# Kernel optimization log

Hardware: AMD Instinct MI355X
Metric: run time of the kernel (lower is better)

The kernel has to match this reference:

```python
import jax, jax.numpy as jnp
import numpy as np

S, N, D, F, E = 2048, 8, 1024, 4096, 8
STD = 0.02


def setup_inputs() -> dict:
    key = jax.random.key(0)
    ks = jax.random.split(key, 5)
    x = jax.random.normal(ks[0], (S, N, D), dtype=jnp.float32)
    Wg = jax.random.normal(ks[1], (E, D), dtype=jnp.float32) * STD
    W1 = jax.random.normal(ks[2], (E, F, D), dtype=jnp.float32) * STD
    b1 = jnp.zeros((E, F), dtype=jnp.float32)
    W2 = jax.random.normal(ks[3], (E, D, F), dtype=jnp.float32) * STD
    b2 = jnp.zeros((E, D), dtype=jnp.float32)
    return {"x": x, "Wg": Wg, "W1": W1, "b1": b1, "W2": W2, "b2": b2}


def reference(x, Wg, W1, b1, W2, b2):
    # Gate (eval mode: no gating noise). scores: [S, N, E]
    scores = jnp.einsum('snd,ed->sne', x, Wg)
    prob = jax.nn.softmax(scores, axis=-1)
    top1_idx = jnp.argmax(prob, axis=-1)                                   # [S, N] int
    top1_prob = jnp.take_along_axis(prob, top1_idx[..., None], axis=-1)[..., 0]  # [S, N]

    y = jnp.zeros_like(x)
    n_experts = Wg.shape[0]
    for e in range(n_experts):  # small fixed loop over experts
        h = jax.nn.gelu(jnp.einsum('snd,fd->snf', x, W1[e]) + b1[e], approximate=False)
        ye = jnp.einsum('snf,df->snd', h, W2[e]) + b2[e]
        mask = (top1_idx == e)[..., None]                                  # [S, N, 1]
        y = y + jnp.where(mask, ye * top1_prob[..., None], 0.0)
    return y
```

## Files before the change

### kernel.cpp

```cpp
#include <hip/hip_runtime.h>

#define S_TOK 16384
#define D_DIM 1024
#define F_DIM 4096
#define E_NUM 8

#define BM 128
#define BN 128
#define BK 64
#define MT_MAX 136

typedef short bf16x8 __attribute__((ext_vector_type(8)));
typedef float f32x4 __attribute__((ext_vector_type(4)));
typedef unsigned short ushort_t;

static __device__ __forceinline__ unsigned short f32_bf16(float f) {
  unsigned u = __float_as_uint(f);
  return (unsigned short)((u + 0x7FFFu + ((u >> 16) & 1u)) >> 16);
}

static __device__ __forceinline__ unsigned int pack_bf16x2(float a, float b) {
  unsigned ua = __float_as_uint(a);
  unsigned ub = __float_as_uint(b);
  unsigned lo = (ua + 0x7FFFu + ((ua >> 16) & 1u)) >> 16;
  unsigned hi = (ub + 0x7FFFu + ((ub >> 16) & 1u)) & 0xFFFF0000u;
  return lo | hi;
}

static __device__ __forceinline__ uint2 cvt_f4_bf4(const float4 v) {
  uint2 r;
  r.x = pack_bf16x2(v.x, v.y);
  r.y = pack_bf16x2(v.z, v.w);
  return r;
}

static __device__ __forceinline__ void load_lds16(const void* g, void* l) {
  __builtin_amdgcn_global_load_lds(g, l, 16, 0, 0);
}

static __device__ __forceinline__ float gelu_f(float v) {
  const float u = fabsf(v) * 0.70710678118654752f;
  const float t = 1.0f / (1.0f + 0.3275911f * u);
  const float poly = t * (0.254829592f + t * (-0.284496736f + t * (1.421413741f +
                     t * (-1.453152027f + t * 1.061405429f))));
  const float erfa = 1.0f - poly * __expf(-u * u);
  const float erfv = (v >= 0.0f) ? erfa : -erfa;
  return 0.5f * v * (1.0f + erfv);
}

__global__ void zero_counts_kernel(int* counts) {
  if (threadIdx.x < E_NUM) counts[threadIdx.x] = 0;
}

__global__ void cast2_kernel(const float* __restrict__ w1, ushort_t* __restrict__ o1,
                             const float* __restrict__ w2, ushort_t* __restrict__ o2) {
  const int half = 16384;
  const float* src = (blockIdx.x < half) ? w1 : w2;
  ushort_t* dst = (blockIdx.x < half) ? o1 : o2;
  const int b = (blockIdx.x < half) ? blockIdx.x : (blockIdx.x - half);
  const size_t base = ((size_t)b * blockDim.x + threadIdx.x) * 8;
  const float4 v0 = *(const float4*)(src + base);
  const float4 v1 = *(const float4*)(src + base + 4);
  const uint2 a = cvt_f4_bf4(v0), c = cvt_f4_bf4(v1);
  uint4 w; w.x = a.x; w.y = a.y; w.z = c.x; w.w = c.y;
  *(uint4*)(dst + base) = w;
}

__global__ void gate_kernel(const float* __restrict__ x,
                            const float* __restrict__ Wg,
                            ushort_t* __restrict__ xbf,
                            float* __restrict__ prob,
                            int* __restrict__ counts,
                            int* __restrict__ tok_list) {
  const int wv = threadIdx.x >> 6;
  const int lane = threadIdx.x & 63;
  const int t = blockIdx.x * 4 + wv;
  const float* xr = x + (size_t)t * D_DIM;
  ushort_t* xb = xbf + (size_t)t * D_DIM;

  float acc[E_NUM];
#pragma unroll
  for (int e = 0; e < E_NUM; ++e) acc[e] = 0.0f;

#pragma unroll
  for (int i = 0; i < 4; ++i) {
    const int k = i * 256 + lane * 4;
    const float4 v = *(const float4*)(xr + k);
    *(uint2*)(xb + k) = cvt_f4_bf4(v);
#pragma unroll
    for (int e = 0; e < E_NUM; ++e) {
      const float4 w = *(const float4*)(Wg + e * D_DIM + k);
      acc[e] += v.x * w.x + v.y * w.y + v.z * w.z + v.w * w.w;
    }
  }
#pragma unroll
  for (int e = 0; e < E_NUM; ++e) {
#pragma unroll
    for (int off = 32; off > 0; off >>= 1)
      acc[e] += __shfl_xor(acc[e], off, 64);
  }
  if (lane == 0) {
    float m = acc[0]; int bi = 0;
#pragma unroll
    for (int e = 1; e < E_NUM; ++e) {
      if (acc[e] > m) { m = acc[e]; bi = e; }
    }
    float s = 0.0f;
#pragma unroll
    for (int e = 0; e < E_NUM; ++e) s += expf(acc[e] - m);
    prob[t] = 1.0f / s;
    int p = atomicAdd(&counts[bi], 1);
    tok_list[bi * S_TOK + p] = t;
  }
}

__global__ void plan_kernel(const int* __restrict__ counts, int* __restrict__ plan) {
  if (threadIdx.x == 0) {
    int t = 0;
    for (int e = 0; e < E_NUM; ++e) {
      const int nt = (counts[e] + BM - 1) / BM;
      for (int i = 0; i < nt; ++i) {
        plan[1 + t] = e;
        plan[1 + MT_MAX + t] = i * BM;
        ++t;
      }
    }
    plan[0] = t;
  }
}

template <int KDIM, int NDIM, int EPI>
__launch_bounds__(256, 2)
__global__ void ffn_kernel(const ushort_t* __restrict__ A,
                           const ushort_t* __restrict__ B,
                           const float* __restrict__ bias,
                           const float* __restrict__ prob,
                           const int* __restrict__ counts,
                           const int* __restrict__ tok_list,
                           const int* __restrict__ plan,
                           ushort_t* __restrict__ Hout,
                           float* __restrict__ out) {
  constexpr int NT = NDIM / BN;
  constexpr int NK = KDIM / BK;
  const int ntiles = plan[0];
  const int live = ntiles * NT;
  if (blockIdx.x >= live) return;
  const int q = live >> 3, r = live & 7;
  const int xcd = blockIdx.x & 7, idx = blockIdx.x >> 3;
  const int wg = (xcd < r ? xcd * (q + 1) : r * (q + 1) + (xcd - r) * q) + idx;
  const int tile = wg / NT;
  const int n0 = (wg % NT) * BN;
  const int e = plan[1 + tile];
  const int m0 = plan[1 + MT_MAX + tile];
  const int cnt = counts[e];

  __shared__ ushort_t As[2][BM * BK];
  __shared__ ushort_t Bs[2][BM * BK];

  const int tid = threadIdx.x;
  const int lane = tid & 63;
  const int w = tid >> 6;
  const int wr = (w >> 1) * 64;
  const int wc = (w & 1) * 64;
  const int l15 = lane & 15;
  const int l4  = lane >> 4;

  const int sub = lane >> 3;
  const int sslot = ((lane & 7) ^ sub) * 8;
  const int dstoff = w * 2048;

  const size_t ebase = (size_t)e * S_TOK;
  const ushort_t* Be = B + (size_t)e * NDIM * KDIM;
  const ushort_t* pA[4];
  const ushort_t* pB[4];
#pragma unroll
  for (int j = 0; j < 4; ++j) {
    const int ra = m0 + w * 32 + j * 8 + sub;
    const int tok = (ra < cnt) ? tok_list[ebase + ra] : 0;
    pA[j] = A + (size_t)tok * KDIM + sslot;
    pB[j] = Be + (size_t)(n0 + w * 32 + j * 8 + sub) * KDIM + sslot;
  }

  int oA[4][2], oB[4][2];
#pragma unroll
  for (int m = 0; m < 4; ++m) {
    const int rr = wr + m * 16 + l15;
#pragma unroll
    for (int kk = 0; kk < 2; ++kk)
      oA[m][kk] = rr * BK + (((kk * 4 + l4) ^ (rr & 7)) * 8);
  }
#pragma unroll
  for (int n = 0; n < 4; ++n) {
    const int rr = wc + n * 16 + l15;
#pragma unroll
    for (int kk = 0; kk < 2; ++kk)
      oB[n][kk] = rr * BK + (((kk * 4 + l4) ^ (rr & 7)) * 8);
  }

  f32x4 acc[4][4];
#pragma unroll
  for (int i = 0; i < 4; ++i)
#pragma unroll
    for (int j = 0; j < 4; ++j)
      acc[i][j] = (f32x4){0.f, 0.f, 0.f, 0.f};

#pragma unroll
  for (int j = 0; j < 4; ++j) {
    load_lds16(pA[j], &As[0][dstoff + j * 512]);
    load_lds16(pB[j], &Bs[0][dstoff + j * 512]);
  }
  __syncthreads();

  int cb = 0;
  for (int t = 0; t < NK; ++t) {
    if (t + 1 < NK) {
      const int k0 = (t + 1) * BK;
      const int nb = cb ^ 1;
#pragma unroll
      for (int j = 0; j < 4; ++j) {
        load_lds16(pA[j] + k0, &As[nb][dstoff + j * 512]);
        load_lds16(pB[j] + k0, &Bs[nb][dstoff + j * 512]);
      }
    }

#pragma unroll
    for (int kk = 0; kk < 2; ++kk) {
      bf16x8 a[4], b[4];
#pragma unroll
      for (int i = 0; i < 4; ++i) {
        a[i] = *(const bf16x8*)&As[cb][oA[i][kk]];
        b[i] = *(const bf16x8*)&Bs[cb][oB[i][kk]];
      }
#pragma unroll
      for (int mi = 0; mi < 4; ++mi)
#pragma unroll
        for (int ni = 0; ni < 4; ++ni)
          acc[mi][ni] = __builtin_amdgcn_mfma_f32_16x16x32_bf16(a[mi], b[ni], acc[mi][ni], 0, 0, 0);
    }

    __syncthreads();
    cb ^= 1;
  }

  const float* be = bias + (size_t)e * NDIM;
#pragma unroll
  for (int mi = 0; mi < 4; ++mi) {
#pragma unroll
    for (int rr = 0; rr < 4; ++rr) {
      const int slot = m0 + wr + mi * 16 + l4 * 4 + rr;
      if (slot >= cnt) continue;
      const int tok = tok_list[ebase + slot];
      if (EPI == 0) {
        ushort_t* hrow = Hout + (size_t)tok * NDIM;
#pragma unroll
        for (int ni = 0; ni < 4; ++ni) {
          const int col = n0 + wc + ni * 16 + l15;
          hrow[col] = f32_bf16(gelu_f(acc[mi][ni][rr] + be[col]));
        }
      } else {
        const float p = prob[tok];
        float* orow = out + (size_t)tok * NDIM;
#pragma unroll
        for (int ni = 0; ni < 4; ++ni) {
          const int col = n0 + wc + ni * 16 + l15;
          orow[col] = (acc[mi][ni][rr] + be[col]) * p;
        }
      }
    }
  }
}

extern "C" void kernel_launch(void* const* d_in, const int* in_sizes, int n_in,
                              void* d_out, int out_size, void* d_ws, size_t ws_size,
                              hipStream_t stream) {
  const float* x  = (const float*)d_in[0];
  const float* Wg = (const float*)d_in[1];
  const float* W1 = (const float*)d_in[2];
  const float* b1 = (const float*)d_in[3];
  const float* W2 = (const float*)d_in[4];
  const float* b2 = (const float*)d_in[5];
  float* out = (float*)d_out;

  const size_t MB = 1ull << 20;
  char* ws = (char*)d_ws;
  int* counts      = (int*)(ws);
  int* plan        = (int*)(ws + 4096);
  float* prob      = (float*)(ws + 64 * 1024);
  int* tok_list    = (int*)(ws + 128 * 1024);
  ushort_t* xbf    = (ushort_t*)(ws + 1 * MB);
  ushort_t* W1bf   = (ushort_t*)(ws + 33 * MB);
  ushort_t* W2bf   = (ushort_t*)(ws + 97 * MB);
  ushort_t* H      = (ushort_t*)(ws + 161 * MB);

  zero_counts_kernel<<<1, 64, 0, stream>>>(counts);
  gate_kernel<<<S_TOK / 4, 256, 0, stream>>>(x, Wg, xbf, prob, counts, tok_list);
  plan_kernel<<<1, 64, 0, stream>>>(counts, plan);

  cast2_kernel<<<32768, 256, 0, stream>>>(W1, W1bf, W2, W2bf);

  ffn_kernel<D_DIM, F_DIM, 0><<<(F_DIM / BN) * MT_MAX, 256, 0, stream>>>(
      xbf, W1bf, b1, nullptr, counts, tok_list, plan, H, nullptr);

  ffn_kernel<F_DIM, D_DIM, 1><<<(D_DIM / BN) * MT_MAX, 256, 0, stream>>>(
      H, W2bf, b2, prob, counts, tok_list, plan, nullptr, out);
}
```

Measured before the change: 831.4 us.

## Load A fragments directly from global into registers, drop A LDS staging

```diff
diff --git a/kernel.cpp b/kernel.cpp
--- a/kernel.cpp
+++ b/kernel.cpp
@@ -130,7 +130,7 @@
 }
 
 template <int KDIM, int NDIM, int EPI>
-__launch_bounds__(256, 2)
+__launch_bounds__(256, 3)
 __global__ void ffn_kernel(const ushort_t* __restrict__ A,
                            const ushort_t* __restrict__ B,
                            const float* __restrict__ bias,
@@ -154,7 +154,6 @@
   const int m0 = plan[1 + MT_MAX + tile];
   const int cnt = counts[e];
 
-  __shared__ ushort_t As[2][BM * BK];
   __shared__ ushort_t Bs[2][BM * BK];
 
   const int tid = threadIdx.x;
@@ -171,24 +170,20 @@
 
   const size_t ebase = (size_t)e * S_TOK;
   const ushort_t* Be = B + (size_t)e * NDIM * KDIM;
-  const ushort_t* pA[4];
   const ushort_t* pB[4];
 #pragma unroll
-  for (int j = 0; j < 4; ++j) {
-    const int ra = m0 + w * 32 + j * 8 + sub;
+  for (int j = 0; j < 4; ++j)
+    pB[j] = Be + (size_t)(n0 + w * 32 + j * 8 + sub) * KDIM + sslot;
+
+  const ushort_t* aP[4];
+#pragma unroll
+  for (int m = 0; m < 4; ++m) {
+    const int ra = m0 + wr + m * 16 + l15;
     const int tok = (ra < cnt) ? tok_list[ebase + ra] : 0;
-    pA[j] = A + (size_t)tok * KDIM + sslot;
-    pB[j] = Be + (size_t)(n0 + w * 32 + j * 8 + sub) * KDIM + sslot;
-  }
-
-  int oA[4][2], oB[4][2];
-#pragma unroll
-  for (int m = 0; m < 4; ++m) {
-    const int rr = wr + m * 16 + l15;
-#pragma unroll
-    for (int kk = 0; kk < 2; ++kk)
-      oA[m][kk] = rr * BK + (((kk * 4 + l4) ^ (rr & 7)) * 8);
-  }
+    aP[m] = A + (size_t)tok * KDIM + l4 * 8;
+  }
+
+  int oB[4][2];
 #pragma unroll
   for (int n = 0; n < 4; ++n) {
     const int rr = wc + n * 16 + l15;
@@ -205,37 +200,39 @@
       acc[i][j] = (f32x4){0.f, 0.f, 0.f, 0.f};
 
 #pragma unroll
-  for (int j = 0; j < 4; ++j) {
-    load_lds16(pA[j], &As[0][dstoff + j * 512]);
+  for (int j = 0; j < 4; ++j)
     load_lds16(pB[j], &Bs[0][dstoff + j * 512]);
-  }
   __syncthreads();
 
   int cb = 0;
   for (int t = 0; t < NK; ++t) {
+    const int k0 = t * BK;
+
+    bf16x8 a[4][2];
+#pragma unroll
+    for (int m = 0; m < 4; ++m)
+#pragma unroll
+      for (int kk = 0; kk < 2; ++kk)
+        a[m][kk] = *(const bf16x8*)(aP[m] + k0 + kk * 32);
+
     if (t + 1 < NK) {
-      const int k0 = (t + 1) * BK;
+      const int kn = (t + 1) * BK;
       const int nb = cb ^ 1;
 #pragma unroll
-      for (int j = 0; j < 4; ++j) {
-        load_lds16(pA[j] + k0, &As[nb][dstoff + j * 512]);
-        load_lds16(pB[j] + k0, &Bs[nb][dstoff + j * 512]);
-      }
+      for (int j = 0; j < 4; ++j)
+        load_lds16(pB[j] + kn, &Bs[nb][dstoff + j * 512]);
     }
 
 #pragma unroll
     for (int kk = 0; kk < 2; ++kk) {
-      bf16x8 a[4], b[4];
-#pragma unroll
-      for (int i = 0; i < 4; ++i) {
-        a[i] = *(const bf16x8*)&As[cb][oA[i][kk]];
-        b[i] = *(const bf16x8*)&Bs[cb][oB[i][kk]];
-      }
+      bf16x8 b[4];
+#pragma unroll
+      for (int n = 0; n < 4; ++n) b[n] = *(const bf16x8*)&Bs[cb][oB[n][kk]];
 #pragma unroll
       for (int mi = 0; mi < 4; ++mi)
 #pragma unroll
         for (int ni = 0; ni < 4; ++ni)
-          acc[mi][ni] = __builtin_amdgcn_mfma_f32_16x16x32_bf16(a[mi], b[ni], acc[mi][ni], 0, 0, 0);
+          acc[mi][ni] = __builtin_amdgcn_mfma_f32_16x16x32_bf16(a[mi][kk], b[ni], acc[mi][ni], 0, 0, 0);
     }
 
     __syncthreads();
```

New measurement: 1.103 ms. 1.33x slower.
